# Optimization experiments

Measured on AMD Instinct MI355X. Metric: run time of the kernel, lower is better.

## Reference

```python
import jax, jax.numpy as jnp
import numpy as np

KS = 3          # image feature patch kernel size
RATE = 2        # downsample rate; alpha patches use kernel RATE*2, stride RATE
PENALTY = -10000.0
EPS = 1e-4
BN_EPS = 1e-5


def _pad(x, k, s):
    # reflect 'same' padding as in GCAModule.pad
    l = (k - s + 1) // 2
    r = (k - s) // 2
    return jnp.pad(x, ((0, 0), (0, 0), (l, r), (l, r)), mode='reflect')


def _extract_patches(x, k, s):
    # replicates reflect-pad + F.unfold + reshape -> (n, L, c, k, k)
    x = _pad(x, k, s)
    n, c, H, W = x.shape
    oh = (H - k) // s + 1
    ow = (W - k) // s + 1
    cols = [x[:, :, di:di + s * (oh - 1) + 1:s, dj:dj + s * (ow - 1) + 1:s]
            for di in range(k) for dj in range(k)]
    p = jnp.stack(cols, axis=2).reshape(n, c, k, k, oh * ow)  # (n,c,k,k,L)
    return jnp.transpose(p, (0, 4, 1, 2, 3))                  # (n,L,c,k,k)


def _deconv(score, kern):
    # torch: F.conv_transpose2d(score[None], kern, stride=RATE, padding=1) / 4
    # score: (L,h,w); kern: (L, ac, 4, 4) in torch conv_transpose (I,O,kh,kw) layout
    k = jnp.transpose(jnp.flip(kern, axis=(2, 3)), (1, 0, 2, 3))  # -> OIHW
    out = jax.lax.conv_general_dilated(
        score[None], k, window_strides=(1, 1), padding=[(2, 2), (2, 2)],
        lhs_dilation=(RATE, RATE), dimension_numbers=('NCHW', 'OIHW', 'NCHW'))
    return out[0] / 4.0


def gca_forward(img_feat, alpha_feat, unknown, gconv_w, gconv_b, oconv_w,
                bn_gamma, bn_beta):
    n = img_feat.shape[0]
    # guidance 1x1 conv + nearest downsample by RATE
    g = jnp.einsum('nchw,oc->nohw', img_feat, gconv_w) + gconv_b[None, :, None, None]
    g = g[:, :, ::RATE, ::RATE]
    u = unknown[:, :, ::RATE, ::RATE]
    # process_unknown_mask: per-sample softmax scales
    um = u.mean(axis=(2, 3))                                    # (n,1)
    km = 1.0 - um
    unknown_scale = jnp.clip(jnp.sqrt(um / km), 0.1, 10.0)      # (n,1)
    known_scale = jnp.clip(jnp.sqrt(km / um), 0.1, 10.0)        # (n,1)
    h, w = g.shape[2], g.shape[3]
    L = h * w
    img_ps = _extract_patches(g, KS, 1)                         # (n,L,c,3,3)
    alpha_ps = _extract_patches(alpha_feat, RATE * 2, RATE)     # (n,L,ac,4,4)
    unk_ps = _extract_patches(u, KS, 1)[:, :, 0].mean(axis=(2, 3))  # (n,L)
    # l2-normalized image patch kernels
    norm = jnp.sqrt(jnp.sum(img_ps * img_ps, axis=(2, 3, 4), keepdims=True))
    img_ps_n = img_ps / jnp.maximum(norm, EPS)
    # similarity: conv of padded g with patch kernels == patches-at-p . kernel-q
    sim = jnp.einsum('npckl,nqckl->nqp', img_ps, img_ps_n)      # (n,L,L)
    is_unknown = (unk_ps > 0.0).astype(sim.dtype)               # (n,L)
    scale = unknown_scale * is_unknown + known_scale * (1.0 - is_unknown)
    out = sim * scale[:, :, None]
    idx = jnp.arange(L)
    out = out.at[:, idx, idx].add(PENALTY * unk_ps)             # self-corr penalty
    gca = jax.nn.softmax(out, axis=1).reshape(n, L, h, w)
    prop = jax.vmap(_deconv)(gca, alpha_ps)                     # (n,ac,2h,2w)
    # out_conv: 1x1 conv (no bias) + BatchNorm (training stats) + residual
    y = jnp.einsum('nchw,oc->nohw', prop, oconv_w)
    mu = y.mean(axis=(0, 2, 3), keepdims=True)
    var = y.var(axis=(0, 2, 3), keepdims=True)
    y = (y - mu) / jnp.sqrt(var + BN_EPS)
    y = y * bn_gamma[None, :, None, None] + bn_beta[None, :, None, None]
    return y + alpha_feat


def setup_inputs():
    key = jax.random.key(0)
    ks = jax.random.split(key, 8)
    N, C, AC, H, W = 4, 256, 128, 64, 64
    img_feat = jax.random.normal(ks[0], (N, C, H, W), jnp.float32)
    alpha_feat = jax.random.normal(ks[1], (N, AC, H, W), jnp.float32)
    unknown = jax.random.randint(ks[2], (N, 1, H, W), 0, 2).astype(jnp.float32)
    gconv_w = jax.random.normal(ks[3], (C // 2, C), jnp.float32) / np.float32(np.sqrt(C))
    gconv_b = jax.random.normal(ks[4], (C // 2,), jnp.float32) * 0.01
    oconv_w = jax.random.normal(ks[5], (AC, AC), jnp.float32) / np.float32(np.sqrt(AC))
    bn_gamma = 0.001 + jax.random.normal(ks[6], (AC,), jnp.float32) * 0.001
    bn_beta = jax.random.normal(ks[7], (AC,), jnp.float32) * 0.001
    return dict(img_feat=img_feat, alpha_feat=alpha_feat, unknown=unknown,
                gconv_w=gconv_w, gconv_b=gconv_b, oconv_w=oconv_w,
                bn_gamma=bn_gamma, bn_beta=bn_beta)


def reference(img_feat, alpha_feat, unknown, gconv_w, gconv_b, oconv_w,
              bn_gamma, bn_beta):
    return gca_forward(img_feat, alpha_feat, unknown, gconv_w, gconv_b,
                       oconv_w, bn_gamma, bn_beta)
```

## Files before the change

kernel.cpp:

```cpp
#include <hip/hip_runtime.h>

#define NN 4
#define CIN 256
#define CH 128
#define HH 64
#define hh 32
#define L 1024
#define NB 2048
#define PENALTY -10000.0f
#define EPS 1e-4f

typedef __bf16 bf16x8 __attribute__((ext_vector_type(8)));
typedef float f32x4 __attribute__((ext_vector_type(4)));
typedef __attribute__((address_space(3))) void lds_t;
typedef __attribute__((address_space(1))) const void gbl_t;

__device__ __forceinline__ int refl32(int t) { return t < 0 ? -t : (t > 31 ? 62 - t : t); }
__device__ __forceinline__ int refl64(int t) { return t < 0 ? -t : (t > 63 ? 126 - t : t); }
__device__ __forceinline__ int swz(int k, int row) { return k ^ (((row >> 1) & 3) << 3); }

__global__ __launch_bounds__(256, 2) void k_gemm0(const float* __restrict__ img,
                                                  const float* __restrict__ gw,
                                                  const float* __restrict__ gb,
                                                  const float* __restrict__ unknown,
                                                  const float* __restrict__ ow,
                                                  __bf16* __restrict__ gbf,
                                                  __bf16* __restrict__ owb,
                                                  float* __restrict__ unk,
                                                  float* __restrict__ scales,
                                                  float* __restrict__ stats) {
    __shared__ __align__(16) unsigned char RAW[73728];
    int bid = blockIdx.x, t = threadIdx.x;
    if (bid >= 36) {
        for (int e = (bid - 36) * 256 + t; e < 16384; e += 8 * 256) {
            int j = e >> 7, m = e & 127;
            owb[e] = (__bf16)ow[j * 128 + swz(m, j)];
        }
        return;
    }
    if (bid >= 32) {
        if (bid == 32) stats[t] = 0.f;
        int n = bid - 32;
        float* u = (float*)RAW;
        float* red = u + 1024;
        float part = 0.f;
#pragma unroll
        for (int c = 0; c < 4; ++c) {
            int idx = t + c * 256;
            int i = idx >> 5, j = idx & 31;
            float v = unknown[n * 4096 + (2 * i) * HH + 2 * j];
            u[idx] = v;
            part += v;
        }
        red[t] = part;
        __syncthreads();
        for (int s = 128; s > 0; s >>= 1) {
            if (t < s) red[t] += red[t + s];
            __syncthreads();
        }
        if (t == 0) {
            float um = red[0] / 1024.0f;
            float km = 1.0f - um;
            scales[n * 2] = fminf(fmaxf(sqrtf(um / km), 0.1f), 10.0f);
            scales[n * 2 + 1] = fminf(fmaxf(sqrtf(km / um), 0.1f), 10.0f);
        }
#pragma unroll
        for (int c = 0; c < 4; ++c) {
            int idx = t + c * 256;
            int i = idx >> 5, j = idx & 31;
            float sum = 0.f;
#pragma unroll
            for (int di = -1; di <= 1; ++di)
#pragma unroll
                for (int dj = -1; dj <= 1; ++dj)
                    sum += u[refl32(i + di) * 32 + refl32(j + dj)];
            unk[n * L + idx] = sum * (1.0f / 9.0f);
        }
        return;
    }
    __bf16* Bfull = (__bf16*)RAW;
    __bf16* As = (__bf16*)(RAW + 65536);
    int p0 = bid * 128;
    int n = bid >> 3;
    int ib = (bid & 7) << 2;
    int l = t & 63, w = t >> 6;
    int wr = w >> 1, wc = w & 1;
#pragma unroll
    for (int it = 0; it < 16; ++it) {
        int fg = it * 256 + t;
        int o = fg >> 5, sg = fg & 31;
        const float* src = gw + o * 256 + sg * 8;
        __bf16 v[8];
#pragma unroll
        for (int e = 0; e < 8; ++e) v[e] = (__bf16)src[e];
        int cs = sg >> 2, lg = sg & 3;
        int dg = lg ^ ((o >> 1) & 3);
        *(bf16x8*)(Bfull + o * 256 + (cs * 4 + dg) * 8) = *(bf16x8*)v;
    }
    f32x4 acc[4][4] = {};
    for (int k0 = 0; k0 < CIN; k0 += 32) {
#pragma unroll
        for (int gi = 0; gi < 2; ++gi) {
            int row = t & 127;
            int sg = (t >> 7) + gi * 2;
            int i = ib + (row >> 5), j = row & 31;
            int c0 = k0 + sg * 8;
            const float* ip = img + (((size_t)n * CIN + c0) * HH + 2 * i) * HH + 2 * j;
            __bf16 v[8];
#pragma unroll
            for (int e = 0; e < 8; ++e) v[e] = (__bf16)ip[(size_t)e * HH * HH];
            int dg = sg ^ ((row >> 1) & 3);
            *(bf16x8*)(As + row * 32 + dg * 8) = *(bf16x8*)v;
        }
        __syncthreads();
        int gl = l >> 4, r = l & 15;
        bf16x8 av[4], bv[4];
#pragma unroll
        for (int m = 0; m < 4; ++m) {
            int row = wr * 64 + m * 16 + r;
            av[m] = *(const bf16x8*)(As + row * 32 + swz(gl << 3, row));
            int col = wc * 64 + m * 16 + r;
            bv[m] = *(const bf16x8*)(Bfull + col * 256 + k0 + swz(gl << 3, col));
        }
#pragma unroll
        for (int m = 0; m < 4; ++m)
#pragma unroll
            for (int c2 = 0; c2 < 4; ++c2)
                acc[m][c2] = __builtin_amdgcn_mfma_f32_16x16x32_bf16(av[m], bv[c2], acc[m][c2], 0, 0, 0);
        __syncthreads();
    }
    int r = l & 15, hi = l >> 4;
#pragma unroll
    for (int m = 0; m < 4; ++m)
#pragma unroll
        for (int c2 = 0; c2 < 4; ++c2) {
            int o = wc * 64 + c2 * 16 + r;
            float bias = gb[o];
#pragma unroll
            for (int reg = 0; reg < 4; ++reg) {
                int row = p0 + wr * 64 + m * 16 + hi * 4 + reg;
                gbf[((size_t)row << 7) + o] = (__bf16)(acc[m][c2][reg] + bias);
            }
        }
}

__global__ __launch_bounds__(256, 2) void k_gemm1(const __bf16* __restrict__ gbf,
                                                  const float* __restrict__ unk,
                                                  const float* __restrict__ scales,
                                                  const float* __restrict__ alpha,
                                                  float* __restrict__ W,
                                                  __bf16* __restrict__ Bt) {
    __shared__ __align__(16) unsigned char RAW[75008];
    int bid = blockIdx.x, t = threadIdx.x;
    if (bid >= 256) {
        float* sm = (float*)RAW;
        int blk = bid - 256;
        int n = blk >> 7, o = blk & 127;
        const float* ap = alpha + ((size_t)(n * CH + o) << 12);
#pragma unroll
        for (int j = 0; j < 4; ++j) {
            int fi = t + j * 256;
            int row = fi >> 4, c4 = fi & 15;
            float4 v = *(const float4*)(ap + fi * 4);
            float* d = sm + row * 65 + c4 * 4;
            d[0] = v.x; d[1] = v.y; d[2] = v.z; d[3] = v.w;
        }
        __syncthreads();
        __bf16* Bn = Bt + ((size_t)(n * NB) << 10);
#pragma unroll
        for (int gi = 0; gi < 8; ++gi) {
            int g = gi * 256 + t;
            int ab = g >> 7, qg = g & 127;
            int a = ab >> 2, bb = ab & 3;
            int q0 = qg * 8;
            int qi = q0 >> 5, qj0 = q0 & 31;
            int ti = refl64(2 * qi + a - 1);
            const float* r = sm + ti * 65;
            __bf16 v[8];
#pragma unroll
            for (int s = 0; s < 8; ++s) v[s] = (__bf16)r[refl64(2 * (qj0 + s) + bb - 1)];
            int j = ab * 128 + o;
            *(bf16x8*)(Bn + ((size_t)j << 10) + swz(q0, j)) = *(bf16x8*)v;
        }
        return;
    }
    __bf16* As1 = (__bf16*)RAW;
    __bf16* Bh = (__bf16*)(RAW + 49152);
    float* ssq = (float*)(RAW + 73728);
    float* ftile = ssq + 192;
    int n = bid >> 6;
    int yy = (bid >> 3) & 7, xx = bid & 7;
    int p0 = yy * 128, q0 = xx * 128;
    const __bf16* gn = gbf + ((size_t)n << 17);
    int l = t & 63, w = t >> 6;
    int wr = w >> 1, wc = w & 1;
    int by4 = yy * 4, bx4 = xx * 4;
    int rbA = by4 - 1; rbA = rbA < 0 ? 0 : (rbA > 26 ? 26 : rbA);
    int rbB = bx4 - 1; rbB = rbB < 0 ? 0 : (rbB > 26 ? 26 : rbB);
#pragma unroll
    for (int k = 0; k < 12; ++k) {
        int chunk = k / 3;
        int rem = (k % 3) * 256 + t;
        int wrow = rem >> 2, sg = rem & 3;
        int so = (chunk << 5) + ((sg ^ ((wrow >> 1) & 3)) << 3);
        int grA = ((rbA + (wrow >> 5)) << 5) + (wrow & 31);
        __builtin_amdgcn_global_load_lds((gbl_t*)(gn + (size_t)grA * 128 + so),
                                         (lds_t*)(As1 + chunk * 6144 + rem * 8), 16, 0, 0);
    }
    auto stageB = [&](int h) {
#pragma unroll
        for (int k = 0; k < 6; ++k) {
            int cl = k / 3;
            int cc = 2 * h + cl;
            int rem = (k % 3) * 256 + t;
            int wrow = rem >> 2, sg = rem & 3;
            int so = (cc << 5) + ((sg ^ ((wrow >> 1) & 3)) << 3);
            int grB = ((rbB + (wrow >> 5)) << 5) + (wrow & 31);
            __builtin_amdgcn_global_load_lds((gbl_t*)(gn + (size_t)grB * 128 + so),
                                             (lds_t*)(Bh + cl * 6144 + rem * 8), 16, 0, 0);
        }
    };
    stageB(0);
    int gl = l >> 4, r = l & 15;
    int rpA_[4][3], cpA_[4][3], rpB_[4][3], cpB_[4][3];
#pragma unroll
    for (int m = 0; m < 4; ++m) {
        int prow = wr * 64 + m * 16 + r;
        int qrow = wc * 64 + m * 16 + r;
#pragma unroll
        for (int d = 0; d < 3; ++d) {
            rpA_[m][d] = (refl32(by4 + (prow >> 5) + d - 1) - rbA) << 10;
            int cp = refl32((prow & 31) + d - 1);
            cpA_[m][d] = cp * 32 + ((gl ^ ((cp >> 1) & 3)) << 3);
            rpB_[m][d] = (refl32(bx4 + (qrow >> 5) + d - 1) - rbB) << 10;
            int cq = refl32((qrow & 31) + d - 1);
            cpB_[m][d] = cq * 32 + ((gl ^ ((cq >> 1) & 3)) << 3);
        }
    }
    f32x4 acc[4][4] = {};
    float ssqAcc = 0.f;
    auto computeH = [&](int h) {
        __builtin_amdgcn_s_setprio(1);
#pragma unroll
        for (int dk = 0; dk < 3; ++dk)
#pragma unroll
            for (int dl = 0; dl < 3; ++dl)
#pragma unroll
                for (int c = 0; c < 2; ++c) {
                    int cc = 2 * h + c;
                    bf16x8 av[4], bv[4];
#pragma unroll
                    for (int m = 0; m < 4; ++m) {
                        av[m] = *(const bf16x8*)(As1 + cc * 6144 + rpA_[m][dk] + cpA_[m][dl]);
                        bv[m] = *(const bf16x8*)(Bh + c * 6144 + rpB_[m][dk] + cpB_[m][dl]);
                    }
#pragma unroll
                    for (int m = 0; m < 4; ++m)
#pragma unroll
                        for (int c2 = 0; c2 < 4; ++c2)
                            acc[m][c2] = __builtin_amdgcn_mfma_f32_16x16x32_bf16(av[m], bv[c2], acc[m][c2], 0, 0, 0);
                }
        __builtin_amdgcn_s_setprio(0);
        if (t < 192) {
            int key = (t >> 1) & 3;
#pragma unroll
            for (int c = 0; c < 2; ++c)
#pragma unroll
                for (int g = 0; g < 4; ++g) {
                    bf16x8 v = *(const bf16x8*)(Bh + c * 6144 + t * 32 + ((g ^ key) << 3));
#pragma unroll
                    for (int u2 = 0; u2 < 8; ++u2) {
                        float x = (float)v[u2];
                        ssqAcc += x * x;
                    }
                }
        }
    };
    __syncthreads();
    computeH(0);
    __syncthreads();
    stageB(1);
    __syncthreads();
    computeH(1);
    if (t < 192) ssq[t] = ssqAcc;
    __syncthreads();
    if (t < 128) {
        int q = q0 + t;
        int qi = q >> 5, qj = q & 31;
        float sum = 0.f;
#pragma unroll
        for (int di = -1; di <= 1; ++di)
#pragma unroll
            for (int dj = -1; dj <= 1; ++dj)
                sum += ssq[(refl32(qi + di) - rbB) * 32 + refl32(qj + dj)];
        float sc = unk[n * L + q] > 0.f ? scales[n * 2] : scales[n * 2 + 1];
        ftile[t] = sc / fmaxf(sqrtf(sum), EPS);
    }
    __syncthreads();
    int hi = l >> 4;
#pragma unroll
    for (int m = 0; m < 4; ++m)
#pragma unroll
        for (int c2 = 0; c2 < 4; ++c2) {
            int q = q0 + wc * 64 + c2 * 16 + r;
            float fq = ftile[wc * 64 + c2 * 16 + r];
#pragma unroll
            for (int reg = 0; reg < 4; ++reg) {
                int p = p0 + wr * 64 + m * 16 + hi * 4 + reg;
                float val = acc[m][c2][reg] * fq;
                if (p == q) val += PENALTY * unk[n * L + p];
                W[((size_t)n << 20) + ((size_t)p << 10) + q] = val;
            }
        }
}

__global__ void k_softmax(const float* __restrict__ W, __bf16* __restrict__ Wb) {
    int t = threadIdx.x, wv = t >> 6, lane = t & 63;
    int row = blockIdx.x * 4 + wv;
    const float4* Wr4 = (const float4*)(W + (size_t)row * 1024);
    float4 v[4];
    float mx = -1e30f;
#pragma unroll
    for (int k = 0; k < 4; ++k) {
        v[k] = Wr4[lane + k * 64];
        mx = fmaxf(mx, fmaxf(fmaxf(v[k].x, v[k].y), fmaxf(v[k].z, v[k].w)));
    }
#pragma unroll
    for (int off = 32; off > 0; off >>= 1) mx = fmaxf(mx, __shfl_xor(mx, off));
    float sum = 0.f;
#pragma unroll
    for (int k = 0; k < 4; ++k) {
        v[k].x = __expf(v[k].x - mx);
        v[k].y = __expf(v[k].y - mx);
        v[k].z = __expf(v[k].z - mx);
        v[k].w = __expf(v[k].w - mx);
        sum += (v[k].x + v[k].y) + (v[k].z + v[k].w);
    }
#pragma unroll
    for (int off = 32; off > 0; off >>= 1) sum += __shfl_xor(sum, off);
    float inv = 1.0f / sum;
    int p = row & (L - 1);
    int key = ((p >> 1) & 3) << 3;
    __bf16* Wbr = Wb + (size_t)row * 1024;
#pragma unroll
    for (int k = 0; k < 4; ++k) {
        int base = 4 * lane + 256 * k;
        __bf16 o4[4];
        o4[0] = (__bf16)(v[k].x * inv);
        o4[1] = (__bf16)(v[k].y * inv);
        o4[2] = (__bf16)(v[k].z * inv);
        o4[3] = (__bf16)(v[k].w * inv);
        __bf16* dst = Wbr + (base ^ key);
        *(uint*)dst = *(uint*)&o4[0];
        *(uint*)(dst + 2) = *(uint*)&o4[2];
    }
}

__global__ __launch_bounds__(256, 2) void k_gemm2(const __bf16* __restrict__ Wb,
                                                  const __bf16* __restrict__ Bt,
                                                  __bf16* __restrict__ Tb) {
    int bid = blockIdx.x;
    int xcd = bid & 7, idx = bid >> 3;
    int n = xcd >> 1;
    int p0 = ((xcd & 1) * 4 + (idx & 3)) * 128;
    int j0 = (idx >> 2) * 128;
    __shared__ __align__(16) __bf16 As[4][4096];
    __shared__ __align__(16) __bf16 Bs[4][4096];
    const __bf16* An = Wb + ((size_t)n << 20);
    const __bf16* Bn = Bt + ((size_t)n * NB << 10);
    int t = threadIdx.x, l = t & 63, w = t >> 6;
    int wr = w >> 1, wc = w & 1;
    int gl = l >> 4, r = l & 15;
    f32x4 acc[4][4] = {};

    auto stage = [&](int buf, int k0) {
#pragma unroll
        for (int i = 0; i < 2; ++i) {
            int row = (t >> 2) + i * 64;
            int sgo = (t & 3) * 8;
            const __bf16* srcA = An + ((size_t)(p0 + row) << 10) + k0 + sgo;
            __builtin_amdgcn_global_load_lds((gbl_t*)srcA, (lds_t*)(&As[buf][row * 32 + sgo]), 16, 0, 0);
            const __bf16* srcB = Bn + ((size_t)(j0 + row) << 10) + k0 + sgo;
            __builtin_amdgcn_global_load_lds((gbl_t*)srcB, (lds_t*)(&Bs[buf][row * 32 + sgo]), 16, 0, 0);
        }
    };
    auto compute = [&](int buf) {
        bf16x8 av[4], bv[4];
#pragma unroll
        for (int m = 0; m < 4; ++m) {
            int row = wr * 64 + m * 16 + r;
            av[m] = *(const bf16x8*)(&As[buf][row * 32 + ((gl ^ ((row >> 1) & 3)) << 3)]);
            int col = wc * 64 + m * 16 + r;
            bv[m] = *(const bf16x8*)(&Bs[buf][col * 32 + ((gl ^ ((col >> 1) & 3)) << 3)]);
        }
#pragma unroll
        for (int m = 0; m < 4; ++m)
#pragma unroll
            for (int c2 = 0; c2 < 4; ++c2)
                acc[m][c2] = __builtin_amdgcn_mfma_f32_16x16x32_bf16(av[m], bv[c2], acc[m][c2], 0, 0, 0);
    };

    stage(0, 0);
    stage(1, 32);
    for (int it = 0; it < 32; ++it) {
        int buf = it & 3;
        if (it + 2 < 32) stage((it + 2) & 3, (it + 2) * 32);
        if (it < 30)
            asm volatile("s_waitcnt vmcnt(8)\n\ts_barrier" ::: "memory");
        else if (it == 30)
            asm volatile("s_waitcnt vmcnt(4)\n\ts_barrier" ::: "memory");
        else
            asm volatile("s_waitcnt vmcnt(0)\n\ts_barrier" ::: "memory");
        compute(buf);
    }
    int hi = l >> 4;
#pragma unroll
    for (int m = 0; m < 4; ++m)
#pragma unroll
        for (int c2 = 0; c2 < 4; ++c2) {
            int j = j0 + wc * 64 + c2 * 16 + r;
#pragma unroll
            for (int reg = 0; reg < 4; ++reg) {
                int p = p0 + wr * 64 + m * 16 + hi * 4 + reg;
                Tb[((size_t)n * L + p) * NB + j] = (__bf16)acc[m][c2][reg];
            }
        }
}

__global__ void k_oconv(const __bf16* __restrict__ owb, const __bf16* __restrict__ Tb,
                        float* __restrict__ y2, float* __restrict__ stats) {
    __shared__ __align__(16) __bf16 As[4 * 4096];
    __shared__ __align__(16) __bf16 Bp[4 * 2048];
    int n = blockIdx.z;
    int x0 = blockIdx.x * 64;
    int t = threadIdx.x, l = t & 63, w = t >> 6;
    int wr = w >> 1, wc = w & 1;
    int gl = l >> 4, r = l & 15, hi = l >> 4;
#pragma unroll
    for (int c = 0; c < 4; ++c)
#pragma unroll
        for (int i = 0; i < 2; ++i) {
            int h = i * 256 + t;
            const __bf16* src = owb + (size_t)(h >> 2) * CH + c * 32 + (h & 3) * 8;
            __builtin_amdgcn_global_load_lds((gbl_t*)src, (lds_t*)(As + c * 4096 + h * 8), 16, 0, 0);
        }
    const __bf16* Tn = Tb + ((size_t)(n * L) << 11);
#pragma unroll
    for (int it = 0; it < 4; ++it) {
        int e2 = it * 256 + t;
        int og = e2 & 15, pl = e2 >> 4;
        int pix = x0 + pl;
        int x = pix & 63, y = pix >> 6;
        float acc8[8] = {};
        int ap = (y + 1) & 1, bp = (x + 1) & 1;
#pragma unroll
        for (int da = 0; da < 2; ++da) {
            int a = ap + 2 * da;
            int ny = y + 1 - a;
            if (ny < 0 || ny >= 64) continue;
            int py = ny >> 1;
#pragma unroll
            for (int db = 0; db < 2; ++db) {
                int bb = bp + 2 * db;
                int nx = x + 1 - bb;
                if (nx < 0 || nx >= 64) continue;
                int px = nx >> 1;
                bf16x8 v = *(const bf16x8*)(Tn + (((size_t)(py * hh + px)) << 11) + (a * 4 + bb) * 128 + og * 8);
#pragma unroll
                for (int u2 = 0; u2 < 8; ++u2) acc8[u2] += (float)v[u2];
            }
        }
        __bf16 rr[8];
#pragma unroll
        for (int u2 = 0; u2 < 8; ++u2) rr[u2] = (__bf16)(acc8[u2] * 0.25f);
        int key = (pix >> 1) & 3;
        int dgl = (og & 3) ^ key;
        *(bf16x8*)(Bp + (og >> 2) * 2048 + pl * 32 + dgl * 8) = *(bf16x8*)rr;
    }
    __syncthreads();
    f32x4 acc[4][2] = {};
#pragma unroll
    for (int c = 0; c < 4; ++c) {
        bf16x8 av[4], bv[2];
#pragma unroll
        for (int m = 0; m < 4; ++m) {
            int row = wr * 64 + m * 16 + r;
            av[m] = *(const bf16x8*)(As + c * 4096 + row * 32 + ((gl ^ ((row >> 1) & 3)) << 3));
        }
#pragma unroll
        for (int c2 = 0; c2 < 2; ++c2) {
            int col = wc * 32 + c2 * 16 + r;
            bv[c2] = *(const bf16x8*)(Bp + c * 2048 + col * 32 + ((gl ^ ((col >> 1) & 3)) << 3));
        }
#pragma unroll
        for (int m = 0; m < 4; ++m)
#pragma unroll
            for (int c2 = 0; c2 < 2; ++c2)
                acc[m][c2] = __builtin_amdgcn_mfma_f32_16x16x32_bf16(av[m], bv[c2], acc[m][c2], 0, 0, 0);
    }
#pragma unroll
    for (int m = 0; m < 4; ++m)
#pragma unroll
        for (int c2 = 0; c2 < 2; ++c2) {
            int pix = x0 + wc * 32 + c2 * 16 + r;
#pragma unroll
            for (int reg = 0; reg < 4; ++reg) {
                int j = wr * 64 + m * 16 + hi * 4 + reg;
                y2[(((size_t)n * CH + j) << 12) + pix] = acc[m][c2][reg];
            }
        }
    __syncthreads();
    float* partS = (float*)As;
    float* partS2 = partS + 256;
#pragma unroll
    for (int m = 0; m < 4; ++m)
#pragma unroll
        for (int reg = 0; reg < 4; ++reg) {
            float s = 0.f, s2 = 0.f;
#pragma unroll
            for (int c2 = 0; c2 < 2; ++c2) {
                float v = acc[m][c2][reg];
                s += v;
                s2 += v * v;
            }
#pragma unroll
            for (int off = 1; off < 16; off <<= 1) {
                s += __shfl_xor(s, off);
                s2 += __shfl_xor(s2, off);
            }
            if (r == 0) {
                int j = wr * 64 + m * 16 + hi * 4 + reg;
                partS[j * 2 + wc] = s;
                partS2[j * 2 + wc] = s2;
            }
        }
    __syncthreads();
    if (t < 128) {
        atomicAdd(&stats[t * 2], partS[t * 2] + partS[t * 2 + 1]);
        atomicAdd(&stats[t * 2 + 1], partS2[t * 2] + partS2[t * 2 + 1]);
    }
}

__global__ void k_final(const float* __restrict__ y2, const float* __restrict__ stats,
                        const float* __restrict__ gamma, const float* __restrict__ beta,
                        const float* __restrict__ alpha, float* __restrict__ out) {
    int e4 = blockIdx.x * 256 + threadIdx.x;
    int oc = (e4 >> 10) & 127;
    float s1 = stats[oc * 2], s2 = stats[oc * 2 + 1];
    float mu = s1 * (1.0f / 16384.0f);
    float var = s2 * (1.0f / 16384.0f) - mu * mu;
    float inv = rsqrtf(var + 1e-5f);
    float g = gamma[oc], b = beta[oc];
    float4 yv = ((const float4*)y2)[e4];
    float4 av = ((const float4*)alpha)[e4];
    float4 o;
    o.x = (yv.x - mu) * inv * g + b + av.x;
    o.y = (yv.y - mu) * inv * g + b + av.y;
    o.z = (yv.z - mu) * inv * g + b + av.z;
    o.w = (yv.w - mu) * inv * g + b + av.w;
    ((float4*)out)[e4] = o;
}

extern "C" void kernel_launch(void* const* d_in, const int* in_sizes, int n_in,
                              void* d_out, int out_size, void* d_ws, size_t ws_size,
                              hipStream_t stream) {
    const float* img = (const float*)d_in[0];
    const float* alpha = (const float*)d_in[1];
    const float* unknown = (const float*)d_in[2];
    const float* gw = (const float*)d_in[3];
    const float* gb = (const float*)d_in[4];
    const float* ow = (const float*)d_in[5];
    const float* gamma = (const float*)d_in[6];
    const float* beta = (const float*)d_in[7];
    float* out = (float*)d_out;
    float* ws = (float*)d_ws;

    __bf16* owb = (__bf16*)(ws + 540672);
    __bf16* gbf = (__bf16*)(ws + 548864);
    float* unk = ws + 815104;
    float* scales = ws + 819200;
    float* stats = ws + 819264;
    float* W = ws + 819520;
    __bf16* Wb = (__bf16*)(ws + 5013824);
    __bf16* Bt = (__bf16*)(ws + 7110976);
    __bf16* Tb = (__bf16*)(ws + 11305280);
    float* y2 = ws + 15499584;

    k_gemm0<<<44, 256, 0, stream>>>(img, gw, gb, unknown, ow, gbf, owb, unk, scales, stats);
    k_gemm1<<<768, 256, 0, stream>>>(gbf, unk, scales, alpha, W, Bt);
    k_softmax<<<1024, 256, 0, stream>>>(W, Wb);
    k_gemm2<<<512, 256, 0, stream>>>(Wb, Bt, Tb);
    k_oconv<<<dim3(64, 1, 4), 256, 0, stream>>>(owb, Tb, y2, stats);
    k_final<<<2048, 256, 0, stream>>>(y2, stats, gamma, beta, alpha, out);
}
```

Before: 91.32 us.

## Stage strided image loads via LDS scratch and stream weight tiles per k-step

The guidance-conv GEMM previously gathered the stride-2 downsampled image with scalar loads strided by a full channel plane, and preloaded the whole 128x256 weight matrix into 64KB of LDS. Now each k-step reads contiguous float4 rows of the image into a padded LDS scratch, keeping every other pixel. It then transposes them into the swizzled bf16 A tile, and loads only the 32-wide weight slice for that step into a small B tile. This cuts LDS from 72KB to about 33KB, which may allow more blocks per CU, and makes global reads coalesced. The cost is an extra barrier per k-step and reading the weight slice repeatedly inside the loop.

After: 101.6 us. 1.11x slower.

```diff
diff --git a/kernel.cpp b/kernel.cpp
--- a/kernel.cpp
+++ b/kernel.cpp
@@ -29,7 +29,7 @@
                                                   float* __restrict__ unk,
                                                   float* __restrict__ scales,
                                                   float* __restrict__ stats) {
-    __shared__ __align__(16) unsigned char RAW[73728];
+    __shared__ __align__(16) unsigned char RAW[33792];
     int bid = blockIdx.x, t = threadIdx.x;
     if (bid >= 36) {
         for (int e = (bid - 36) * 256 + t; e < 16384; e += 8 * 256) {
@@ -78,49 +78,58 @@
         }
         return;
     }
-    __bf16* Bfull = (__bf16*)RAW;
-    __bf16* As = (__bf16*)(RAW + 65536);
+    float* scr = (float*)RAW;
+    __bf16* As = (__bf16*)(RAW + 16896);
+    __bf16* Bs = (__bf16*)(RAW + 25088);
     int p0 = bid * 128;
     int n = bid >> 3;
     int ib = (bid & 7) << 2;
     int l = t & 63, w = t >> 6;
     int wr = w >> 1, wc = w & 1;
-#pragma unroll
-    for (int it = 0; it < 16; ++it) {
-        int fg = it * 256 + t;
-        int o = fg >> 5, sg = fg & 31;
-        const float* src = gw + o * 256 + sg * 8;
-        __bf16 v[8];
-#pragma unroll
-        for (int e = 0; e < 8; ++e) v[e] = (__bf16)src[e];
-        int cs = sg >> 2, lg = sg & 3;
-        int dg = lg ^ ((o >> 1) & 3);
-        *(bf16x8*)(Bfull + o * 256 + (cs * 4 + dg) * 8) = *(bf16x8*)v;
-    }
+    int gl = l >> 4, r = l & 15;
     f32x4 acc[4][4] = {};
     for (int k0 = 0; k0 < CIN; k0 += 32) {
 #pragma unroll
-        for (int gi = 0; gi < 2; ++gi) {
-            int row = t & 127;
-            int sg = (t >> 7) + gi * 2;
-            int i = ib + (row >> 5), j = row & 31;
-            int c0 = k0 + sg * 8;
-            const float* ip = img + (((size_t)n * CIN + c0) * HH + 2 * i) * HH + 2 * j;
+        for (int it = 0; it < 8; ++it) {
+            int task = it * 256 + t;
+            int j2 = task & 15;
+            int ci = task >> 4;
+            int c = ci >> 2, i = ci & 3;
+            const float* ip = img + (((size_t)n * CIN + k0 + c) * HH + 2 * (ib + i)) * HH + 4 * j2;
+            float4 v = *(const float4*)ip;
+            scr[ci * 33 + 2 * j2] = v.x;
+            scr[ci * 33 + 2 * j2 + 1] = v.z;
+        }
+        __syncthreads();
+#pragma unroll
+        for (int it = 0; it < 2; ++it) {
+            int task = it * 256 + t;
+            int row = task >> 2, g = task & 3;
+            int i = row >> 5, j = row & 31;
+            int key = (row >> 1) & 3;
             __bf16 v[8];
 #pragma unroll
-            for (int e = 0; e < 8; ++e) v[e] = (__bf16)ip[(size_t)e * HH * HH];
-            int dg = sg ^ ((row >> 1) & 3);
-            *(bf16x8*)(As + row * 32 + dg * 8) = *(bf16x8*)v;
+            for (int s = 0; s < 8; ++s) {
+                int ch = s ^ g;
+                v[ch] = (__bf16)scr[((g * 8 + ch) * 4 + i) * 33 + j];
+            }
+            *(bf16x8*)(As + row * 32 + ((g ^ key) << 3)) = *(bf16x8*)v;
+            const float* src = gw + row * 256 + k0 + g * 8;
+            float4 b0 = *(const float4*)src;
+            float4 b1 = *(const float4*)(src + 4);
+            __bf16 bv[8];
+            bv[0] = (__bf16)b0.x; bv[1] = (__bf16)b0.y; bv[2] = (__bf16)b0.z; bv[3] = (__bf16)b0.w;
+            bv[4] = (__bf16)b1.x; bv[5] = (__bf16)b1.y; bv[6] = (__bf16)b1.z; bv[7] = (__bf16)b1.w;
+            *(bf16x8*)(Bs + row * 32 + ((g ^ key) << 3)) = *(bf16x8*)bv;
         }
         __syncthreads();
-        int gl = l >> 4, r = l & 15;
         bf16x8 av[4], bv[4];
 #pragma unroll
         for (int m = 0; m < 4; ++m) {
             int row = wr * 64 + m * 16 + r;
             av[m] = *(const bf16x8*)(As + row * 32 + swz(gl << 3, row));
             int col = wc * 64 + m * 16 + r;
-            bv[m] = *(const bf16x8*)(Bfull + col * 256 + k0 + swz(gl << 3, col));
+            bv[m] = *(const bf16x8*)(Bs + col * 32 + swz(gl << 3, col));
         }
 #pragma unroll
         for (int m = 0; m < 4; ++m)
@@ -129,7 +138,7 @@
                 acc[m][c2] = __builtin_amdgcn_mfma_f32_16x16x32_bf16(av[m], bv[c2], acc[m][c2], 0, 0, 0);
         __syncthreads();
     }
-    int r = l & 15, hi = l >> 4;
+    int hi = l >> 4;
 #pragma unroll
     for (int m = 0; m < 4; ++m)
 #pragma unroll
```
